# Kernel optimization log

Measured on AMD Instinct MI355X. Metric: run time of the kernel, lower is better.

Reference implementation:

```python
import jax, jax.numpy as jnp
import numpy as np

B, L, D = 2, 2048, 1024
H, K = 16, 16
HD = D // H


def setup_inputs() -> dict:
    key = jax.random.key(0)
    k1, k2, k3, k4, k5 = jax.random.split(key, 5)
    x = jax.random.normal(k1, (B, L, D), dtype=jnp.float32)
    # Linear weight (out_features, in_features), small init to keep logits sane
    w_in = jax.random.normal(k2, (3 * D, D), dtype=jnp.float32) * 0.02
    # TISA radial-basis kernel parameters, per (head, kernel)
    kernel_offsets = jax.random.normal(k3, (H, K), dtype=jnp.float32) * 20.0
    kernel_amplitudes = 0.1 + 0.01 * jax.random.normal(k4, (H, K), dtype=jnp.float32)
    kernel_sharpness = 0.1 + 0.01 * jax.random.normal(k5, (H, K), dtype=jnp.float32)
    return {"x": x, "w_in": w_in, "kernel_offsets": kernel_offsets,
            "kernel_amplitudes": kernel_amplitudes, "kernel_sharpness": kernel_sharpness}


def tisa_bias(offsets, amplitudes, sharpness, seq_len):
    # relative positions -(L-1) .. (L-1)  -> per-head RBF positional scores
    rel = jnp.arange(-(seq_len - 1), seq_len, dtype=jnp.float32)  # (2L-1,)
    # scores[h, m] = sum_k amp[h,k] * exp(-|sharp[h,k]| * (off[h,k] - rel[m])^2)
    diff = offsets[:, :, None] - rel[None, None, :]               # (H, K, 2L-1)
    scores = jnp.sum(amplitudes[:, :, None] * jnp.exp(-jnp.abs(sharpness)[:, :, None] * diff * diff), axis=1)  # (H, 2L-1)
    # Toeplitz expansion: bias[h, i, j] = scores[h, (i - j) + (L-1)]
    i = jnp.arange(seq_len)
    idx = i[:, None] - i[None, :] + (seq_len - 1)                 # (L, L)
    return scores[:, idx]                                         # (H, L, L)


def reference(x, w_in, kernel_offsets, kernel_amplitudes, kernel_sharpness):
    b, l, d = x.shape
    proj = jnp.einsum('bld,ed->ble', x, w_in)                     # (B, L, 3D)
    # split: memory = first 2D (k then v), query = last D
    k_, v_, q_ = proj[..., :d], proj[..., d:2 * d], proj[..., 2 * d:]

    def heads(t):
        return t.reshape(b, l, H, HD).transpose(0, 2, 1, 3)       # (B, H, L, HD)

    q, k, v = heads(q_), heads(k_), heads(v_)
    bias = tisa_bias(kernel_offsets, kernel_amplitudes, kernel_sharpness, l)  # (H, L, L)
    scale = 1.0 / np.sqrt(HD).astype(np.float32)
    logits = jnp.einsum('bhld,bhmd->bhlm', q, k) * scale + bias[None]
    attn = jax.nn.softmax(logits, axis=-1)
    out = jnp.einsum('bhlm,bhmd->bhld', attn, v)                  # (B, H, L, HD)
    return out.transpose(0, 2, 1, 3).reshape(b, l, d)             # (B, L, D)
```

## Files before the change

### kernel.cpp

```cpp
#include <hip/hip_runtime.h>
#include <hip/hip_bf16.h>
#include <stdint.h>
#include <stddef.h>


#define NB     2
#define NH     16
#define SL     2048
#define DH     64
#define DMODEL 1024
#define SCP    4096
#define LOG2E  1.44269504088896340736f

typedef __attribute__((ext_vector_type(8)))  short bf16x8;
typedef __attribute__((ext_vector_type(4)))  short bf16x4;
typedef __attribute__((ext_vector_type(4)))  float f32x4;
typedef __attribute__((ext_vector_type(16))) float f32x16;

static __device__ __forceinline__ short f2bf(float x) {
  __hip_bfloat16 h = __float2bfloat16(x);
  return *reinterpret_cast<short*>(&h);
}
static __device__ __forceinline__ short f2bf_fast(float x) {
  union { float f; uint32_t u; } v; v.f = x;
  return (short)((v.u + 0x8000u) >> 16);
}
static __device__ __forceinline__ long long bf4_to_ll(bf16x4 v) {
  long long r; __builtin_memcpy(&r, &v, 8); return r;
}
static __device__ __forceinline__ bf16x4 ll_to_bf4(long long v) {
  bf16x4 r; __builtin_memcpy(&r, &v, 8); return r;
}
static __device__ __forceinline__ float fexp2(float x) {
#if __has_builtin(__builtin_amdgcn_exp2f)
  return __builtin_amdgcn_exp2f(x);
#else
  return __expf(x * 0.69314718056f);
#endif
}
#define GLD(g, l) __builtin_amdgcn_global_load_lds( \
    (const __attribute__((address_space(1))) void*)(g), \
    (__attribute__((address_space(3))) void*)(l), 16, 0, 0)

__global__ __launch_bounds__(256) void prep_k(
    const float* __restrict__ x, const float* __restrict__ w,
    const float* __restrict__ koff, const float* __restrict__ kamp,
    const float* __restrict__ kshp,
    short* __restrict__ xbf, short* __restrict__ wbf,
    float* __restrict__ scores) {
  const int bx = blockIdx.x, tid = threadIdx.x;
  if (bx < 7168) {
    const float* src = (bx < 4096) ? x : w;
    short* dst       = (bx < 4096) ? xbf : wbf;
    const int i      = (bx < 4096 ? bx : bx - 4096) * 256 + tid;
    float4 a = *(const float4*)(src + (size_t)i * 4);
    bf16x4 o;
    o.x = f2bf(a.x); o.y = f2bf(a.y); o.z = f2bf(a.z); o.w = f2bf(a.w);
    *(bf16x4*)(dst + (size_t)i * 4) = o;
  } else {
    const int idx = bx - 7168;
    const int h = idx >> 4;
    const int r = (idx & 15) * 256 + tid;
    if (r >= 4095) return;
    float rel = (float)(r - (SL - 1));
    float acc = 0.f;
#pragma unroll
    for (int k = 0; k < 16; ++k) {
      float o = koff[h * 16 + k];
      float a = kamp[h * 16 + k];
      float s = fabsf(kshp[h * 16 + k]);
      float d = o - rel;
      acc += a * __expf(-s * d * d);
    }
    scores[h * SCP + r] = acc * LOG2E;
  }
}

__global__ __launch_bounds__(256) void qkv_gemm_k(
    const short* __restrict__ A, const short* __restrict__ Bw,
    __hip_bfloat16* __restrict__ kbuf, __hip_bfloat16* __restrict__ vbufT,
    __hip_bfloat16* __restrict__ qbuf) {
  __shared__ __align__(16) short SM[12288];
  short* As = SM;
  short* Bs = SM + 8192;
  const int tid  = threadIdx.x;
  const int lane = tid & 63;
  const int wv   = tid >> 6;
  const int l15  = lane & 15, quad = lane >> 4;
  const int wm = (wv & 1) * 64, wn = (wv >> 1) * 32;
  const int xt = blockIdx.x, yt = blockIdx.y;
  const int m0 = yt * 128, n0 = xt * 64;
  const int which = xt >> 4;
  const int hh    = xt & 15;

  f32x4 acc[4][2];
#pragma unroll
  for (int r = 0; r < 4; ++r)
#pragma unroll
    for (int c = 0; c < 2; ++c) acc[r][c] = (f32x4){0.f, 0.f, 0.f, 0.f};

  for (int kt = 0; kt < 16; ++kt) {
    const int k0 = kt * 64;
#pragma unroll
    for (int it = 0; it < 4; ++it) {
      const int e8  = it * 256 + tid;
      GLD(A + (size_t)(m0 + (e8 >> 3)) * DMODEL + k0 + (e8 & 7) * 8, &As[e8 * 8]);
    }
#pragma unroll
    for (int it = 0; it < 2; ++it) {
      const int e8  = it * 256 + tid;
      GLD(Bw + (size_t)(n0 + (e8 >> 3)) * DMODEL + k0 + (e8 & 7) * 8, &Bs[e8 * 8]);
    }
    __syncthreads();
#pragma unroll
    for (int ki = 0; ki < 64; ki += 32) {
      bf16x8 af[4], bfv[2];
#pragma unroll
      for (int r = 0; r < 4; ++r)
        af[r] = *(const bf16x8*)&As[(wm + r * 16 + l15) * 64 + ki + quad * 8];
#pragma unroll
      for (int c = 0; c < 2; ++c)
        bfv[c] = *(const bf16x8*)&Bs[(wn + c * 16 + l15) * 64 + ki + quad * 8];
#pragma unroll
      for (int r = 0; r < 4; ++r)
#pragma unroll
        for (int c = 0; c < 2; ++c)
          acc[r][c] = __builtin_amdgcn_mfma_f32_16x16x32_bf16(af[r], bfv[c], acc[r][c], 0, 0, 0);
    }
    __syncthreads();
  }

  const int bb  = m0 >> 11;
  const int llb = m0 & 2047;
  if (which != 1) {
    const float qs = (which == 2) ? 0.125f * LOG2E : 1.0f;
#pragma unroll
    for (int r = 0; r < 4; ++r)
#pragma unroll
      for (int c = 0; c < 2; ++c)
#pragma unroll
        for (int gg = 0; gg < 4; ++gg)
          SM[(wm + r * 16 + quad * 4 + gg) * 72 + wn + c * 16 + l15] =
              f2bf_fast(acc[r][c][gg] * qs);
    __syncthreads();
    __hip_bfloat16* dst = (which == 0) ? kbuf : qbuf;
#pragma unroll
    for (int i = 0; i < 4; ++i) {
      const int cidx = i * 256 + tid;
      const int m = cidx >> 3, ch = cidx & 7;
      bf16x8 val = *(const bf16x8*)&SM[m * 72 + ch * 8];
      *(bf16x8*)&dst[(((size_t)bb * NH + hh) * SL + llb + m) * DH + ch * 8] = val;
    }
  } else {
#pragma unroll
    for (int r = 0; r < 4; ++r)
#pragma unroll
      for (int c = 0; c < 2; ++c) {
        bf16x4 pk;
#pragma unroll
        for (int gg = 0; gg < 4; ++gg) pk[gg] = f2bf_fast(acc[r][c][gg]);
        *(bf16x4*)&SM[(wn + c * 16 + l15) * 136 + wm + r * 16 + quad * 4] = pk;
      }
    __syncthreads();
#pragma unroll
    for (int i = 0; i < 4; ++i) {
      const int cidx = i * 256 + tid;
      const int n = cidx >> 4, ch = cidx & 15;
      bf16x8 val = *(const bf16x8*)&SM[n * 136 + ch * 8];
      *(bf16x8*)&vbufT[(((size_t)bb * NH + hh) * DH + n) * SL + llb + ch * 8] = val;
    }
  }
}

__global__ __launch_bounds__(256, 4) void attn_k(
    const __hip_bfloat16* __restrict__ qbuf, const __hip_bfloat16* __restrict__ kbuf,
    const __hip_bfloat16* __restrict__ vbufT, const float* __restrict__ scores,
    float* __restrict__ out) {
  __shared__ __align__(16) short Ks[2][64 * 72];
  __shared__ __align__(16) short Vs[2][64 * 72];
  __shared__ __align__(16) float Bt[2][128];
  const int bh   = blockIdx.x;
  const int b    = bh >> 4, h = bh & 15;
  const int tid  = threadIdx.x;
  const int lane = tid & 63;
  const int w    = tid >> 6;
  const int wv   = w & 1;
  const int kw   = w >> 1;
  const int n32  = lane & 31, hf = lane >> 5;
  const int i0b  = blockIdx.y * 64;
  const int i0   = i0b + wv * 32;
  const __hip_bfloat16* qb = qbuf + (size_t)bh * SL * DH;
  const short* kb = (const short*)(kbuf + (size_t)bh * SL * DH);
  const short* vb = (const short*)(vbufT + (size_t)bh * DH * SL);
  const float* sc = scores + h * SCP;

  bf16x8 qf[4];
#pragma unroll
  for (int kc = 0; kc < 4; ++kc)
    qf[kc] = *(const bf16x8*)&qb[(size_t)(i0 + n32) * DH + kc * 16 + hf * 8];

  f32x16 ot[2];
#pragma unroll
  for (int dt = 0; dt < 2; ++dt)
#pragma unroll
    for (int r = 0; r < 16; ++r) ot[dt][r] = 0.f;
  float ls[4] = {0.f, 0.f, 0.f, 0.f};

  auto stage = [&](int bsel, int j0) {
    const short* ksrc = kb + (size_t)j0 * DH;
#pragma unroll
    for (int i = 0; i < 2; ++i) {
      int c = i * 256 + tid; int r = c / 9, s = c - r * 9;
      GLD(ksrc + (size_t)r * DH + s * 8, &Ks[bsel][c * 8]);
    }
    if (tid < 64) {
      int c = 512 + tid; int r = c / 9, s = c - r * 9;
      GLD(ksrc + (size_t)r * DH + s * 8, &Ks[bsel][c * 8]);
    }
#pragma unroll
    for (int i = 0; i < 2; ++i) {
      int c = i * 256 + tid; int r = c / 9, s = c - r * 9;
      GLD(vb + (size_t)r * SL + j0 + s * 8, &Vs[bsel][c * 8]);
    }
    if (tid < 64) {
      int c = 512 + tid; int r = c / 9, s = c - r * 9;
      GLD(vb + (size_t)r * SL + j0 + s * 8, &Vs[bsel][c * 8]);
    }
    if (tid < 32) GLD(sc + (i0b - j0 + 1984) + tid * 4, &Bt[bsel][tid * 4]);
  };

  auto compute = [&](int bsel) {
    const short* Kp = Ks[bsel];
    const short* Vp = Vs[bsel];
    const float* Bp = Bt[bsel];
    f32x16 st;
    const int tb0 = wv * 32 + n32 - kw * 32 - 4 * hf + 63;
#pragma unroll
    for (int g = 0; g < 4; ++g)
#pragma unroll
      for (int i = 0; i < 4; ++i) st[g * 4 + i] = Bp[tb0 - 8 * g - i];
    __builtin_amdgcn_s_setprio(1);
#pragma unroll
    for (int kc = 0; kc < 4; ++kc) {
      bf16x8 kf = *(const bf16x8*)&Kp[(kw * 32 + n32) * 72 + kc * 16 + hf * 8];
      st = __builtin_amdgcn_mfma_f32_32x32x16_bf16(kf, qf[kc], st, 0, 0, 0);
    }
    __builtin_amdgcn_s_setprio(0);
    bf16x4 pk[4];
#pragma unroll
    for (int g = 0; g < 4; ++g)
#pragma unroll
      for (int i = 0; i < 4; ++i) {
        const float p = fexp2(st[g * 4 + i]);
        ls[g] += p;
        pk[g][i] = f2bf_fast(p);
      }
    long long s0 = hf ? bf4_to_ll(pk[0]) : bf4_to_ll(pk[1]);
    bf16x4 r0 = ll_to_bf4(__shfl_xor(s0, 32));
    bf16x8 pf0 = hf == 0 ? __builtin_shufflevector(pk[0], r0, 0, 1, 2, 3, 4, 5, 6, 7)
                         : __builtin_shufflevector(r0, pk[1], 0, 1, 2, 3, 4, 5, 6, 7);
    long long s1 = hf ? bf4_to_ll(pk[2]) : bf4_to_ll(pk[3]);
    bf16x4 r1 = ll_to_bf4(__shfl_xor(s1, 32));
    bf16x8 pf1 = hf == 0 ? __builtin_shufflevector(pk[2], r1, 0, 1, 2, 3, 4, 5, 6, 7)
                         : __builtin_shufflevector(r1, pk[3], 0, 1, 2, 3, 4, 5, 6, 7);
    __builtin_amdgcn_s_setprio(1);
#pragma unroll
    for (int dt = 0; dt < 2; ++dt) {
      const short* vr = &Vp[(dt * 32 + n32) * 72 + kw * 32];
      bf16x8 vf0 = *(const bf16x8*)&vr[hf * 8];
      bf16x8 vf1 = *(const bf16x8*)&vr[16 + hf * 8];
      ot[dt] = __builtin_amdgcn_mfma_f32_32x32x16_bf16(vf0, pf0, ot[dt], 0, 0, 0);
      ot[dt] = __builtin_amdgcn_mfma_f32_32x32x16_bf16(vf1, pf1, ot[dt], 0, 0, 0);
    }
    __builtin_amdgcn_s_setprio(0);
  };

  stage(0, 0);
  __syncthreads();
  int cur = 0;
  for (int j0 = 64; j0 < SL; j0 += 64) {
    stage(cur ^ 1, j0);
    compute(cur);
    __syncthreads();
    cur ^= 1;
  }
  compute(cur);
  __syncthreads();

  float lsum = (ls[0] + ls[1]) + (ls[2] + ls[3]);
  lsum += __shfl_xor(lsum, 32);
  float* red = (float*)&Ks[0][0];
  const int rbase = (wv * 64 + lane) * 36;
  if (kw == 1) {
#pragma unroll
    for (int dt = 0; dt < 2; ++dt)
#pragma unroll
      for (int g = 0; g < 4; ++g) {
        f32x4 v;
#pragma unroll
        for (int i = 0; i < 4; ++i) v[i] = ot[dt][g * 4 + i];
        *(f32x4*)&red[rbase + dt * 16 + g * 4] = v;
      }
    red[rbase + 32] = lsum;
  }
  __syncthreads();
  if (kw == 0) {
#pragma unroll
    for (int dt = 0; dt < 2; ++dt)
#pragma unroll
      for (int g = 0; g < 4; ++g) {
        f32x4 v = *(const f32x4*)&red[rbase + dt * 16 + g * 4];
#pragma unroll
        for (int i = 0; i < 4; ++i) ot[dt][g * 4 + i] += v[i];
      }
    lsum += red[rbase + 32];
    const float inv = 1.f / lsum;
    float* orow = out + (((size_t)b * SL + i0 + n32) * NH + h) * DH;
#pragma unroll
    for (int dt = 0; dt < 2; ++dt)
#pragma unroll
      for (int g = 0; g < 4; ++g) {
        f32x4 v;
#pragma unroll
        for (int i = 0; i < 4; ++i) v[i] = ot[dt][g * 4 + i] * inv;
        *(f32x4*)&orow[dt * 32 + 8 * g + 4 * hf] = v;
      }
  }
}

extern "C" void kernel_launch(void* const* d_in, const int* in_sizes, int n_in,
                              void* d_out, int out_size, void* d_ws, size_t ws_size,
                              hipStream_t stream) {
  const float* x    = (const float*)d_in[0];
  const float* w    = (const float*)d_in[1];
  const float* koff = (const float*)d_in[2];
  const float* kamp = (const float*)d_in[3];
  const float* kshp = (const float*)d_in[4];
  float* out = (float*)d_out;

  const size_t per = (size_t)NB * NH * SL * DH;
  const size_t nx  = (size_t)NB * SL * DMODEL;
  const size_t nw  = (size_t)3 * DMODEL * DMODEL;

  __hip_bfloat16* kbuf  = (__hip_bfloat16*)d_ws;
  __hip_bfloat16* vbufT = kbuf + per;
  __hip_bfloat16* qbuf  = vbufT + per;
  float* scores = (float*)(qbuf + per);
  short* xbf    = (short*)(scores + (size_t)NH * SCP);
  short* wbf    = xbf + nx;

  prep_k<<<7424, 256, 0, stream>>>(x, w, koff, kamp, kshp, xbf, wbf, scores);
  qkv_gemm_k<<<dim3(48, 32), 256, 0, stream>>>(xbf, wbf, kbuf, vbufT, qbuf);
  attn_k<<<dim3(NB * NH, SL / 64), 256, 0, stream>>>(qbuf, kbuf, vbufT, scores, out);
}
```

Baseline: 179.5 us.

## Widen attention blocks to 128 query rows with 8 waves sharing K/V tiles

The attention kernel now launches 512-thread blocks covering 128 query rows (four query-wave groups times two key-split groups), so each staged K/V tile in shared memory is reused by twice as many waves and grid size halves. The staging loads are redistributed across the larger thread count, the bias window grows to 192 entries, and the cross-wave reduction is split between the K and V shared buffers. Separately, the prep conversion kernel processes 8 floats per thread instead of 4. The trade-off is fewer blocks (512) and a larger block footprint, which may reduce occupancy and latency hiding.

Measured after the change: 174.4 us. -2.8%, faster.

```diff
diff --git a/kernel.cpp b/kernel.cpp
--- a/kernel.cpp
+++ b/kernel.cpp
@@ -49,16 +49,18 @@
     short* __restrict__ xbf, short* __restrict__ wbf,
     float* __restrict__ scores) {
   const int bx = blockIdx.x, tid = threadIdx.x;
-  if (bx < 7168) {
-    const float* src = (bx < 4096) ? x : w;
-    short* dst       = (bx < 4096) ? xbf : wbf;
-    const int i      = (bx < 4096 ? bx : bx - 4096) * 256 + tid;
-    float4 a = *(const float4*)(src + (size_t)i * 4);
-    bf16x4 o;
-    o.x = f2bf(a.x); o.y = f2bf(a.y); o.z = f2bf(a.z); o.w = f2bf(a.w);
-    *(bf16x4*)(dst + (size_t)i * 4) = o;
+  if (bx < 3584) {
+    const float* src = (bx < 2048) ? x : w;
+    short* dst       = (bx < 2048) ? xbf : wbf;
+    const size_t i   = ((size_t)(bx < 2048 ? bx : bx - 2048) * 256 + tid) * 8;
+    float4 a = *(const float4*)(src + i);
+    float4 b = *(const float4*)(src + i + 4);
+    bf16x8 o;
+    o[0] = f2bf(a.x); o[1] = f2bf(a.y); o[2] = f2bf(a.z); o[3] = f2bf(a.w);
+    o[4] = f2bf(b.x); o[5] = f2bf(b.y); o[6] = f2bf(b.z); o[7] = f2bf(b.w);
+    *(bf16x8*)(dst + i) = o;
   } else {
-    const int idx = bx - 7168;
+    const int idx = bx - 3584;
     const int h = idx >> 4;
     const int r = (idx & 15) * 256 + tid;
     if (r >= 4095) return;
@@ -172,22 +174,22 @@
   }
 }
 
-__global__ __launch_bounds__(256, 4) void attn_k(
+__global__ __launch_bounds__(512, 4) void attn_k(
     const __hip_bfloat16* __restrict__ qbuf, const __hip_bfloat16* __restrict__ kbuf,
     const __hip_bfloat16* __restrict__ vbufT, const float* __restrict__ scores,
     float* __restrict__ out) {
   __shared__ __align__(16) short Ks[2][64 * 72];
   __shared__ __align__(16) short Vs[2][64 * 72];
-  __shared__ __align__(16) float Bt[2][128];
+  __shared__ __align__(16) float Bt[2][192];
   const int bh   = blockIdx.x;
   const int b    = bh >> 4, h = bh & 15;
   const int tid  = threadIdx.x;
   const int lane = tid & 63;
   const int w    = tid >> 6;
-  const int wv   = w & 1;
-  const int kw   = w >> 1;
+  const int wv   = w & 3;
+  const int kw   = w >> 2;
   const int n32  = lane & 31, hf = lane >> 5;
-  const int i0b  = blockIdx.y * 64;
+  const int i0b  = blockIdx.y * 128;
   const int i0   = i0b + wv * 32;
   const __hip_bfloat16* qb = qbuf + (size_t)bh * SL * DH;
   const short* kb = (const short*)(kbuf + (size_t)bh * SL * DH);
@@ -208,25 +210,23 @@
 
   auto stage = [&](int bsel, int j0) {
     const short* ksrc = kb + (size_t)j0 * DH;
-#pragma unroll
-    for (int i = 0; i < 2; ++i) {
-      int c = i * 256 + tid; int r = c / 9, s = c - r * 9;
+    {
+      int c = tid; int r = c / 9, s = c - r * 9;
       GLD(ksrc + (size_t)r * DH + s * 8, &Ks[bsel][c * 8]);
     }
     if (tid < 64) {
       int c = 512 + tid; int r = c / 9, s = c - r * 9;
       GLD(ksrc + (size_t)r * DH + s * 8, &Ks[bsel][c * 8]);
     }
-#pragma unroll
-    for (int i = 0; i < 2; ++i) {
-      int c = i * 256 + tid; int r = c / 9, s = c - r * 9;
+    {
+      int c = tid; int r = c / 9, s = c - r * 9;
       GLD(vb + (size_t)r * SL + j0 + s * 8, &Vs[bsel][c * 8]);
     }
     if (tid < 64) {
       int c = 512 + tid; int r = c / 9, s = c - r * 9;
       GLD(vb + (size_t)r * SL + j0 + s * 8, &Vs[bsel][c * 8]);
     }
-    if (tid < 32) GLD(sc + (i0b - j0 + 1984) + tid * 4, &Bt[bsel][tid * 4]);
+    if (tid < 48) GLD(sc + (i0b - j0 + 1984) + tid * 4, &Bt[bsel][tid * 4]);
   };
 
   auto compute = [&](int bsel) {
@@ -289,8 +289,9 @@
 
   float lsum = (ls[0] + ls[1]) + (ls[2] + ls[3]);
   lsum += __shfl_xor(lsum, 32);
-  float* red = (float*)&Ks[0][0];
-  const int rbase = (wv * 64 + lane) * 36;
+  float* red = (wv < 2)
+      ? (float*)&Ks[0][0] + ((wv * 64 + lane) * 36)
+      : (float*)&Vs[0][0] + (((wv - 2) * 64 + lane) * 36);
   if (kw == 1) {
 #pragma unroll
     for (int dt = 0; dt < 2; ++dt)
@@ -299,9 +300,9 @@
         f32x4 v;
 #pragma unroll
         for (int i = 0; i < 4; ++i) v[i] = ot[dt][g * 4 + i];
-        *(f32x4*)&red[rbase + dt * 16 + g * 4] = v;
-      }
-    red[rbase + 32] = lsum;
+        *(f32x4*)&red[dt * 16 + g * 4] = v;
+      }
+    red[32] = lsum;
   }
   __syncthreads();
   if (kw == 0) {
@@ -309,11 +310,11 @@
     for (int dt = 0; dt < 2; ++dt)
 #pragma unroll
       for (int g = 0; g < 4; ++g) {
-        f32x4 v = *(const f32x4*)&red[rbase + dt * 16 + g * 4];
+        f32x4 v = *(const f32x4*)&red[dt * 16 + g * 4];
 #pragma unroll
         for (int i = 0; i < 4; ++i) ot[dt][g * 4 + i] += v[i];
       }
-    lsum += red[rbase + 32];
+    lsum += red[32];
     const float inv = 1.f / lsum;
     float* orow = out + (((size_t)b * SL + i0 + n32) * NH + h) * DH;
 #pragma unroll
@@ -349,7 +350,7 @@
   short* xbf    = (short*)(scores + (size_t)NH * SCP);
   short* wbf    = xbf + nx;
 
-  prep_k<<<7424, 256, 0, stream>>>(x, w, koff, kamp, kshp, xbf, wbf, scores);
+  prep_k<<<3840, 256, 0, stream>>>(x, w, koff, kamp, kshp, xbf, wbf, scores);
   qkv_gemm_k<<<dim3(48, 32), 256, 0, stream>>>(xbf, wbf, kbuf, vbufT, qbuf);
-  attn_k<<<dim3(NB * NH, SL / 64), 256, 0, stream>>>(qbuf, kbuf, vbufT, scores, out);
-}
+  attn_k<<<dim3(NB * NH, SL / 128), 512, 0, stream>>>(qbuf, kbuf, vbufT, scores, out);
+}
```
